# Kernel tuning notes

Hardware: AMD Instinct MI355X
Metric: run time of the kernel (lower is better)

Reference implementation:

```python
import jax, jax.numpy as jnp
import numpy as np

C = 256
CQK = C // 8  # 32


def setup_inputs() -> dict:
    key = jax.random.key(0)
    ks = jax.random.split(key, 8)
    B, H, W = 4, 64, 64
    x = jax.random.normal(ks[0], (B, H, W, C), dtype=jnp.float32)
    # 1x1 conv weights == dense projections over channel dim
    Wf = jax.random.normal(ks[1], (C, CQK), dtype=jnp.float32) * (1.0 / np.sqrt(C))
    bf = jnp.zeros((CQK,), dtype=jnp.float32)
    Wg = jax.random.normal(ks[2], (C, CQK), dtype=jnp.float32) * (1.0 / np.sqrt(C))
    bg = jnp.zeros((CQK,), dtype=jnp.float32)
    Wh = jax.random.normal(ks[3], (C, C), dtype=jnp.float32) * (1.0 / np.sqrt(C))
    bh = jnp.zeros((C,), dtype=jnp.float32)
    gamma = jnp.float32(0.5)  # nonzero so attention path contributes
    return {"x": x, "Wf": Wf, "bf": bf, "Wg": Wg, "bg": bg, "Wh": Wh, "bh": bh, "gamma": gamma}


def reference(x, Wf, bf, Wg, bg, Wh, bh, gamma):
    B, H, W, Cc = x.shape
    N = H * W
    xf = x.reshape(B, N, Cc)                       # hw_flatten
    f = xf @ Wf + bf                               # [B, N, C//8] keys
    g = xf @ Wg + bg                               # [B, N, C//8] queries
    h = xf @ Wh + bh                               # [B, N, C] values
    s = jnp.einsum('bnc,bmc->bnm', g, f)           # [B, N, N]
    b = jax.nn.softmax(s, axis=-1)
    o = jnp.einsum('bnm,bmc->bnc', b, h)           # [B, N, C]
    y = gamma * o.reshape(B, H, W, Cc) + x
    return y
```

## Files before the change

### kernel.cpp

```cpp
#include <hip/hip_runtime.h>
#include <hip/hip_bf16.h>

#define BATCH 4
#define NSEQ  4096
#define CDIM  256
#define CQK   32
#define L2E   1.44269504088896340736f

typedef short bf16x8 __attribute__((ext_vector_type(8)));
typedef float f32x16 __attribute__((ext_vector_type(16)));
typedef unsigned short u16;
typedef unsigned int   u32;
typedef unsigned int   u32x4 __attribute__((ext_vector_type(4)));

__device__ __forceinline__ u32 pk2(float lo, float hi) {
  u16 a = __builtin_bit_cast(u16, __float2bfloat16(lo));
  u16 b = __builtin_bit_cast(u16, __float2bfloat16(hi));
  return (u32)a | ((u32)b << 16);
}
__device__ __forceinline__ bf16x8 ld8(const u16* p) {
  uint4 u = *(const uint4*)p;
  return __builtin_bit_cast(bf16x8, u);
}
__device__ __forceinline__ float exp2_raw(float x) {
#if __has_builtin(__builtin_amdgcn_exp2f)
  return __builtin_amdgcn_exp2f(x);
#else
  return exp2f(x);
#endif
}

__global__ __launch_bounds__(64) void prep_kernel(
    const float* __restrict__ Wf, const float* __restrict__ Wg, const float* __restrict__ Wh,
    u16* __restrict__ wfT, u16* __restrict__ wgT, u16* __restrict__ whT) {
  const int cb = blockIdx.x, t = threadIdx.x;
#pragma unroll
  for (int j = 0; j < 4; ++j) {
    const int k = t + j * 64;
    if (cb < 32) {
      wfT[cb * 256 + k] = (u16)(pk2(Wf[k * CQK + cb] * L2E, 0.f) & 0xFFFF);
    } else if (cb < 64) {
      const int c = cb - 32;
      wgT[c * 256 + k] = (u16)(pk2(Wg[k * CQK + c], 0.f) & 0xFFFF);
    } else {
      const int c = cb - 64;
      whT[c * 256 + k] = (u16)(pk2(Wh[k * CDIM + c], 0.f) & 0xFFFF);
    }
  }
}

__global__ __launch_bounds__(256, 1) void proj_kernel(
    const float* __restrict__ x,
    const float* __restrict__ bfv, const float* __restrict__ bgv, const float* __restrict__ bhv,
    const u16* __restrict__ wfT, const u16* __restrict__ wgT, const u16* __restrict__ whT,
    u16* __restrict__ f_ws, u16* __restrict__ g_ws, u16* __restrict__ hT_ws) {
  const int tid   = threadIdx.x;
  const int lan   = tid & 63;
  const int lan31 = lan & 31;
  const int g2    = lan >> 5;
  const int w     = tid >> 6;
  const int half  = w >> 1;
  const int row0  = blockIdx.x * 64 + (w & 1) * 32;
  const int b     = row0 >> 12, n0 = row0 & (NSEQ - 1);

  bf16x8 xf[16];
  const float* xr = x + ((size_t)row0 + lan31) * CDIM + g2 * 8;
#pragma unroll
  for (int ks = 0; ks < 16; ++ks) {
    float4 a = *(const float4*)(xr + ks * 16);
    float4 c = *(const float4*)(xr + ks * 16 + 4);
    u32x4 u = { pk2(a.x, a.y), pk2(a.z, a.w), pk2(c.x, c.y), pk2(c.z, c.w) };
    xf[ks] = __builtin_bit_cast(bf16x8, u);
  }

  {
    const u16*  wT   = half ? wgT : wfT;
    const float bias = half ? bgv[lan31] : bfv[lan31] * L2E;
    f32x16 acc;
#pragma unroll
    for (int r = 0; r < 16; ++r) acc[r] = bias;
    const u16* wp = wT + lan31 * 256 + g2 * 8;
#pragma unroll
    for (int ks = 0; ks < 16; ++ks)
      acc = __builtin_amdgcn_mfma_f32_32x32x16_bf16(xf[ks], ld8(wp + ks * 16), acc, 0, 0, 0);
    u16* dst = half ? g_ws : f_ws;
#pragma unroll
    for (int r = 0; r < 16; ++r) {
      const int row = (r & 3) + 8 * (r >> 2) + 4 * g2;
      dst[((size_t)row0 + row) * CQK + lan31] = (u16)(pk2(acc[r], 0.f) & 0xFFFF);
    }
  }

#pragma unroll
  for (int t = 0; t < 4; ++t) {
    const int ct = half * 128 + t * 32;
    f32x16 acc;
#pragma unroll
    for (int r = 0; r < 16; ++r)
      acc[r] = bhv[ct + (r & 3) + 8 * (r >> 2) + 4 * g2];
    const u16* wp = whT + (size_t)(ct + lan31) * 256 + g2 * 8;
#pragma unroll
    for (int ks = 0; ks < 16; ++ks)
      acc = __builtin_amdgcn_mfma_f32_32x32x16_bf16(ld8(wp + ks * 16), xf[ks], acc, 0, 0, 0);
#pragma unroll
    for (int r = 0; r < 16; ++r) {
      const int c = ct + (r & 3) + 8 * (r >> 2) + 4 * g2;
      hT_ws[((size_t)b * CDIM + c) * NSEQ + n0 + lan31] = (u16)(pk2(acc[r], 0.f) & 0xFFFF);
    }
  }
}

__global__ __launch_bounds__(512, 2) void attn_kernel(
    const float* __restrict__ x, const float* __restrict__ gamma_p,
    const u16* __restrict__ f_ws, const u16* __restrict__ g_ws,
    const u16* __restrict__ hT_ws, float* __restrict__ out) {
  __shared__ u32x4 xb[2][4][4][2][64];
  __shared__ u32   pls[4][2][2][16][64];
  __shared__ float lsh[4][4][64];

  const int tid   = threadIdx.x;
  const int lan   = tid & 63;
  const int lan31 = lan & 31;
  const int g2    = lan >> 5;
  const int w     = tid >> 6;
  const int kw    = w & 3;
  const int cq    = w >> 2;
  const int bid   = blockIdx.x;
  const int xcd   = bid & 7;
  const int b     = xcd >> 1;
  const int inner = bid >> 3;
  const int cb    = inner & 1;
  const int n0    = (((xcd & 1) << 4) | (inner >> 1)) * 128;

  const float gamma = gamma_p[0];

  bf16x8 bgM[2][2];
#pragma unroll
  for (int qhl = 0; qhl < 2; ++qhl) {
    const u16* gp = g_ws + ((size_t)b * NSEQ + n0 + (cq * 2 + qhl) * 32 + lan31) * CQK + g2 * 8;
    bgM[qhl][0] = ld8(gp);
    bgM[qhl][1] = ld8(gp + 16);
  }

  f32x16 o[2][4], zfrag;
#pragma unroll
  for (int r = 0; r < 16; ++r) zfrag[r] = 0.f;
#pragma unroll
  for (int cg = 0; cg < 2; ++cg)
#pragma unroll
    for (int qh = 0; qh < 4; ++qh) o[cg][qh] = zfrag;
  float l2[2] = {0.f, 0.f};

  const u16* fbase = f_ws + ((size_t)b * NSEQ + kw * 1024 + lan31) * CQK + g2 * 8;
  const u16* hbase = hT_ws + ((size_t)b * CDIM + cb * 128 + cq * 64 + lan31) * NSEQ
                   + kw * 1024 + g2 * 8;

  bf16x8 af0 = ld8(fbase), af1 = ld8(fbase + 16);
  const u16* fp = fbase + 32 * CQK;

  for (int it = 0; it < 32; ++it) {
    const int p = it & 1;
    bf16x8 naf0 = ld8(fp), naf1 = ld8(fp + 16);
    fp += 32 * CQK;
    const u16* hp = hbase + it * 32;
    bf16x8 ha0 = ld8(hp);
    bf16x8 hb0 = ld8(hp + 16);
    bf16x8 ha1 = ld8(hp + (size_t)32 * NSEQ);
    bf16x8 hb1 = ld8(hp + (size_t)32 * NSEQ + 16);

#pragma unroll
    for (int qhl = 0; qhl < 2; ++qhl) {
      f32x16 s = __builtin_amdgcn_mfma_f32_32x32x16_bf16(af0, bgM[qhl][0], zfrag, 0, 0, 0);
      s        = __builtin_amdgcn_mfma_f32_32x32x16_bf16(af1, bgM[qhl][1], s,     0, 0, 0);

      float pv[16];
#pragma unroll
      for (int r = 0; r < 16; ++r) pv[r] = exp2_raw(s[r]);
      float rs = ((pv[0]+pv[1])+(pv[2]+pv[3])) + ((pv[4]+pv[5])+(pv[6]+pv[7]))
               + ((pv[8]+pv[9])+(pv[10]+pv[11])) + ((pv[12]+pv[13])+(pv[14]+pv[15]));
      auto rr = __builtin_amdgcn_permlane32_swap(__builtin_bit_cast(u32, rs),
                                                 __builtin_bit_cast(u32, rs), false, false);
      l2[qhl] += __builtin_bit_cast(float, (u32)rr[0]) + __builtin_bit_cast(float, (u32)rr[1]);

      u32 q0a = pk2(pv[0],pv[1]),   q0b = pk2(pv[2],pv[3]);
      u32 q1a = pk2(pv[4],pv[5]),   q1b = pk2(pv[6],pv[7]);
      u32 q2a = pk2(pv[8],pv[9]),   q2b = pk2(pv[10],pv[11]);
      u32 q3a = pk2(pv[12],pv[13]), q3b = pk2(pv[14],pv[15]);
      auto r02a = __builtin_amdgcn_permlane32_swap(q0a, q1a, false, false);
      auto r13a = __builtin_amdgcn_permlane32_swap(q0b, q1b, false, false);
      auto r02b = __builtin_amdgcn_permlane32_swap(q2a, q3a, false, false);
      auto r13b = __builtin_amdgcn_permlane32_swap(q2b, q3b, false, false);
      u32x4 u0 = {(u32)r02a[0], (u32)r13a[0], (u32)r02a[1], (u32)r13a[1]};
      u32x4 u1 = {(u32)r02b[0], (u32)r13b[0], (u32)r02b[1], (u32)r13b[1]};
      xb[p][kw][cq * 2 + qhl][0][lan] = u0;
      xb[p][kw][cq * 2 + qhl][1][lan] = u1;
    }

    __syncthreads();

    bf16x8 ap[4][2];
#pragma unroll
    for (int qh = 0; qh < 4; ++qh) {
      ap[qh][0] = __builtin_bit_cast(bf16x8, xb[p][kw][qh][0][lan]);
      ap[qh][1] = __builtin_bit_cast(bf16x8, xb[p][kw][qh][1][lan]);
    }

#pragma unroll
    for (int qh = 0; qh < 4; ++qh) {
      o[0][qh] = __builtin_amdgcn_mfma_f32_32x32x16_bf16(ap[qh][0], ha0, o[0][qh], 0, 0, 0);
      o[0][qh] = __builtin_amdgcn_mfma_f32_32x32x16_bf16(ap[qh][1], hb0, o[0][qh], 0, 0, 0);
      o[1][qh] = __builtin_amdgcn_mfma_f32_32x32x16_bf16(ap[qh][0], ha1, o[1][qh], 0, 0, 0);
      o[1][qh] = __builtin_amdgcn_mfma_f32_32x32x16_bf16(ap[qh][1], hb1, o[1][qh], 0, 0, 0);
    }

    af0 = naf0; af1 = naf1;
  }

  lsh[kw][cq * 2 + 0][lan] = l2[0];
  lsh[kw][cq * 2 + 1][lan] = l2[1];

#pragma unroll
  for (int round = 0; round < 2; ++round) {
    __syncthreads();
    {
#pragma unroll
      for (int qhl = 0; qhl < 2; ++qhl)
#pragma unroll
        for (int r = 0; r < 16; ++r)
          pls[kw][cq][qhl][r][lan] = pk2(o[0][round * 2 + qhl][r], o[1][round * 2 + qhl][r]);
    }
    __syncthreads();
    {
      const int qhl = kw & 1, rb = (kw >> 1) * 8;
      const int qh  = round * 2 + qhl;
      float e0[8], e1[8];
#pragma unroll
      for (int j = 0; j < 8; ++j) { e0[j] = 0.f; e1[j] = 0.f; }
#pragma unroll
      for (int kk = 0; kk < 4; ++kk)
#pragma unroll
        for (int j = 0; j < 8; ++j) {
          u32 v = pls[kk][cq][qhl][rb + j][lan];
          e0[j] += __builtin_bit_cast(float, v << 16);
          e1[j] += __builtin_bit_cast(float, v & 0xFFFF0000u);
        }
      const float l_tot = lsh[0][qh][lan] + lsh[1][qh][lan]
                        + lsh[2][qh][lan] + lsh[3][qh][lan];
      const float gi = gamma / l_tot;
#pragma unroll
      for (int j = 0; j < 8; ++j) {
        const int r  = rb + j;
        const int nl = (r & 3) + 8 * (r >> 2) + 4 * g2;
        const float gir = __shfl(gi, nl);
        const size_t row = (size_t)b * NSEQ + n0 + qh * 32 + nl;
        const size_t i0 = row * CDIM + cb * 128 + cq * 64 + lan31;
        out[i0]      = fmaf(gir, e0[j], x[i0]);
        out[i0 + 32] = fmaf(gir, e1[j], x[i0 + 32]);
      }
    }
  }
}

extern "C" void kernel_launch(void* const* d_in, const int* in_sizes, int n_in,
                              void* d_out, int out_size, void* d_ws, size_t ws_size,
                              hipStream_t stream) {
  const float* x     = (const float*)d_in[0];
  const float* Wf    = (const float*)d_in[1];
  const float* bf    = (const float*)d_in[2];
  const float* Wg    = (const float*)d_in[3];
  const float* bg    = (const float*)d_in[4];
  const float* Wh    = (const float*)d_in[5];
  const float* bh    = (const float*)d_in[6];
  const float* gamma = (const float*)d_in[7];
  float* out = (float*)d_out;

  u16* hT_ws = (u16*)d_ws;
  u16* f_ws  = hT_ws + (size_t)BATCH * CDIM * NSEQ;
  u16* g_ws  = f_ws  + (size_t)BATCH * NSEQ * CQK;
  u16* wfT   = g_ws  + (size_t)BATCH * NSEQ * CQK;
  u16* wgT   = wfT   + (size_t)CQK * CDIM;
  u16* whT   = wgT   + (size_t)CQK * CDIM;

  hipLaunchKernelGGL(prep_kernel, dim3(320), dim3(64), 0, stream,
                     Wf, Wg, Wh, wfT, wgT, whT);
  hipLaunchKernelGGL(proj_kernel, dim3(256), dim3(256), 0, stream,
                     x, bf, bg, bh, wfT, wgT, whT, f_ws, g_ws, hT_ws);
  hipLaunchKernelGGL(attn_kernel, dim3(256), dim3(512), 0, stream,
                     x, gamma, f_ws, g_ws, hT_ws, out);
}
```

Before: 86.33 us.

## Pre-pack f and h workspaces into MFMA fragment order for contiguous loads

The projection kernel now writes the key (f) and value (h) tensors in a packed layout where each 32-row tile's MFMA operand fragments sit contiguously (lane*8 order). The attention kernel then reads each fragment with fully coalesced 16-byte loads at a linear stride instead of strided row/column reads across NSEQ. This trades more scattered 2-byte stores in the projection kernel for cheaper, contiguous streaming loads in the hot attention loop.

```diff
diff --git a/kernel.cpp b/kernel.cpp
--- a/kernel.cpp
+++ b/kernel.cpp
@@ -53,7 +53,7 @@
     const float* __restrict__ x,
     const float* __restrict__ bfv, const float* __restrict__ bgv, const float* __restrict__ bhv,
     const u16* __restrict__ wfT, const u16* __restrict__ wgT, const u16* __restrict__ whT,
-    u16* __restrict__ f_ws, u16* __restrict__ g_ws, u16* __restrict__ hT_ws) {
+    u16* __restrict__ fP, u16* __restrict__ g_ws, u16* __restrict__ hP) {
   const int tid   = threadIdx.x;
   const int lan   = tid & 63;
   const int lan31 = lan & 31;
@@ -61,7 +61,8 @@
   const int w     = tid >> 6;
   const int half  = w >> 1;
   const int row0  = blockIdx.x * 64 + (w & 1) * 32;
-  const int b     = row0 >> 12, n0 = row0 & (NSEQ - 1);
+  const int b     = row0 >> 12;
+  const int kcg   = row0 >> 5;
 
   bf16x8 xf[16];
   const float* xr = x + ((size_t)row0 + lan31) * CDIM + g2 * 8;
@@ -83,11 +84,20 @@
 #pragma unroll
     for (int ks = 0; ks < 16; ++ks)
       acc = __builtin_amdgcn_mfma_f32_32x32x16_bf16(xf[ks], ld8(wp + ks * 16), acc, 0, 0, 0);
-    u16* dst = half ? g_ws : f_ws;
-#pragma unroll
-    for (int r = 0; r < 16; ++r) {
-      const int row = (r & 3) + 8 * (r >> 2) + 4 * g2;
-      dst[((size_t)row0 + row) * CQK + lan31] = (u16)(pk2(acc[r], 0.f) & 0xFFFF);
+    if (half) {
+#pragma unroll
+      for (int r = 0; r < 16; ++r) {
+        const int row = (r & 3) + 8 * (r >> 2) + 4 * g2;
+        g_ws[((size_t)row0 + row) * CQK + lan31] = (u16)(pk2(acc[r], 0.f) & 0xFFFF);
+      }
+    } else {
+      u16* fb = fP + (size_t)kcg * 1024
+              + (lan31 >> 4) * 512 + ((lan31 >> 3) & 1) * 256 + (lan31 & 7);
+#pragma unroll
+      for (int r = 0; r < 16; ++r) {
+        const int crow = (r & 3) + 8 * (r >> 2) + 4 * g2;
+        fb[crow * 8] = (u16)(pk2(acc[r], 0.f) & 0xFFFF);
+      }
     }
   }
 
@@ -102,18 +112,21 @@
 #pragma unroll
     for (int ks = 0; ks < 16; ++ks)
       acc = __builtin_amdgcn_mfma_f32_32x32x16_bf16(ld8(wp + ks * 16), xf[ks], acc, 0, 0, 0);
+    const int cg = half * 4 + t;
+    u16* hb = hP + ((size_t)(b * 8 + cg) * 128 + ((row0 & (NSEQ - 1)) >> 5)) * 1024
+            + (lan31 >> 4) * 512 + ((lan31 >> 3) & 1) * 256 + (lan31 & 7);
 #pragma unroll
     for (int r = 0; r < 16; ++r) {
-      const int c = ct + (r & 3) + 8 * (r >> 2) + 4 * g2;
-      hT_ws[((size_t)b * CDIM + c) * NSEQ + n0 + lan31] = (u16)(pk2(acc[r], 0.f) & 0xFFFF);
+      const int crow = (r & 3) + 8 * (r >> 2) + 4 * g2;
+      hb[crow * 8] = (u16)(pk2(acc[r], 0.f) & 0xFFFF);
     }
   }
 }
 
 __global__ __launch_bounds__(512, 2) void attn_kernel(
     const float* __restrict__ x, const float* __restrict__ gamma_p,
-    const u16* __restrict__ f_ws, const u16* __restrict__ g_ws,
-    const u16* __restrict__ hT_ws, float* __restrict__ out) {
+    const u16* __restrict__ fP, const u16* __restrict__ g_ws,
+    const u16* __restrict__ hP, float* __restrict__ out) {
   __shared__ u32x4 xb[2][4][4][2][64];
   __shared__ u32   pls[4][2][2][16][64];
   __shared__ float lsh[4][4][64];
@@ -151,22 +164,20 @@
     for (int qh = 0; qh < 4; ++qh) o[cg][qh] = zfrag;
   float l2[2] = {0.f, 0.f};
 
-  const u16* fbase = f_ws + ((size_t)b * NSEQ + kw * 1024 + lan31) * CQK + g2 * 8;
-  const u16* hbase = hT_ws + ((size_t)b * CDIM + cb * 128 + cq * 64 + lan31) * NSEQ
-                   + kw * 1024 + g2 * 8;
-
-  bf16x8 af0 = ld8(fbase), af1 = ld8(fbase + 16);
-  const u16* fp = fbase + 32 * CQK;
+  const u16* fpk  = fP + (size_t)(b * 128 + kw * 32) * 1024 + lan * 8;
+  const u16* hpk0 = hP + ((size_t)(b * 8 + cb * 4 + cq * 2) * 128 + kw * 32) * 1024 + lan * 8;
+  const u16* hpk1 = hpk0 + (size_t)128 * 1024;
+
+  bf16x8 af0 = ld8(fpk), af1 = ld8(fpk + 512);
+  fpk += 1024;
 
   for (int it = 0; it < 32; ++it) {
     const int p = it & 1;
-    bf16x8 naf0 = ld8(fp), naf1 = ld8(fp + 16);
-    fp += 32 * CQK;
-    const u16* hp = hbase + it * 32;
-    bf16x8 ha0 = ld8(hp);
-    bf16x8 hb0 = ld8(hp + 16);
-    bf16x8 ha1 = ld8(hp + (size_t)32 * NSEQ);
-    bf16x8 hb1 = ld8(hp + (size_t)32 * NSEQ + 16);
+    bf16x8 naf0 = ld8(fpk), naf1 = ld8(fpk + 512);
+    fpk += 1024;
+    bf16x8 ha0 = ld8(hpk0), hb0 = ld8(hpk0 + 512);
+    bf16x8 ha1 = ld8(hpk1), hb1 = ld8(hpk1 + 512);
+    hpk0 += 1024; hpk1 += 1024;
 
 #pragma unroll
     for (int qhl = 0; qhl < 2; ++qhl) {
@@ -274,17 +285,17 @@
   const float* gamma = (const float*)d_in[7];
   float* out = (float*)d_out;
 
-  u16* hT_ws = (u16*)d_ws;
-  u16* f_ws  = hT_ws + (size_t)BATCH * CDIM * NSEQ;
-  u16* g_ws  = f_ws  + (size_t)BATCH * NSEQ * CQK;
-  u16* wfT   = g_ws  + (size_t)BATCH * NSEQ * CQK;
-  u16* wgT   = wfT   + (size_t)CQK * CDIM;
-  u16* whT   = wgT   + (size_t)CQK * CDIM;
+  u16* hP   = (u16*)d_ws;
+  u16* fPp  = hP  + (size_t)BATCH * CDIM * NSEQ;
+  u16* g_ws = fPp + (size_t)BATCH * NSEQ * CQK;
+  u16* wfT  = g_ws + (size_t)BATCH * NSEQ * CQK;
+  u16* wgT  = wfT + (size_t)CQK * CDIM;
+  u16* whT  = wgT + (size_t)CQK * CDIM;
 
   hipLaunchKernelGGL(prep_kernel, dim3(320), dim3(64), 0, stream,
                      Wf, Wg, Wh, wfT, wgT, whT);
   hipLaunchKernelGGL(proj_kernel, dim3(256), dim3(256), 0, stream,
-                     x, bf, bg, bh, wfT, wgT, whT, f_ws, g_ws, hT_ws);
+                     x, bf, bg, bh, wfT, wgT, whT, fPp, g_ws, hP);
   hipLaunchKernelGGL(attn_kernel, dim3(256), dim3(512), 0, stream,
-                     x, gamma, f_ws, g_ws, hT_ws, out);
-}
+                     x, gamma, fPp, g_ws, hP, out);
+}
```

New measurement: 82.30 us. -4.7%, faster.
